# Kernel optimization log

Measured on AMD Instinct MI355X. Metric: run time of the kernel, lower is better.

## Reference

```python
import jax, jax.numpy as jnp
import numpy as np

B, T, C, H = 4, 2048, 1024, 16
D = C // H  # head_dim = 64


def setup_inputs() -> dict:
    key = jax.random.key(0)
    k1, k2, k3 = jax.random.split(key, 3)
    x = jax.random.normal(k1, (B, T, C), dtype=jnp.float32)
    w_attn = jax.random.normal(k2, (C, 3 * C), dtype=jnp.float32) * (1.0 / np.sqrt(C))
    b_attn = jnp.zeros((3 * C,), dtype=jnp.float32)
    w_proj = jax.random.normal(k3, (C, C), dtype=jnp.float32) * (1.0 / np.sqrt(C))
    b_proj = jnp.zeros((C,), dtype=jnp.float32)
    return {"x": x, "w_attn": w_attn, "b_attn": b_attn, "w_proj": w_proj, "b_proj": b_proj}


def reference(x, w_attn, b_attn, w_proj, b_proj):
    Bx, Tx, Cx = x.shape
    qkv = x @ w_attn + b_attn                      # (B, T, 3C)
    q, k, v = jnp.split(qkv, 3, axis=2)
    # (B, T, C) -> (B, H, T, D)
    q = q.reshape(Bx, Tx, H, D).transpose(0, 2, 1, 3)
    k = k.reshape(Bx, Tx, H, D).transpose(0, 2, 1, 3)
    v = v.reshape(Bx, Tx, H, D).transpose(0, 2, 1, 3)
    scores = jnp.einsum('bhqd,bhkd->bhqk', q, k) / jnp.sqrt(jnp.float32(D))
    causal = jnp.tril(jnp.ones((Tx, Tx), dtype=bool))
    scores = jnp.where(causal[None, None], scores, jnp.float32(-jnp.inf))
    probs = jax.nn.softmax(scores, axis=-1)
    out = jnp.einsum('bhqk,bhkd->bhqd', probs, v)  # (B, H, T, D)
    out = out.transpose(0, 2, 1, 3).reshape(Bx, Tx, Cx)
    return out @ w_proj + b_proj
```

## Files before the change

### kernel.cpp

```cpp
#include <hip/hip_runtime.h>

#define AS1 __attribute__((address_space(1)))
#define AS3 __attribute__((address_space(3)))

using bf16x8  = __attribute__((ext_vector_type(8))) __bf16;
using floatx4 = __attribute__((ext_vector_type(4))) float;

#define SCQ 0.18033688f

__device__ inline ushort f2b(float f) {
    __bf16 h = (__bf16)f;
    return __builtin_bit_cast(ushort, h);
}

__device__ inline float fexp2(float x) {
    float r;
    asm("v_exp_f32 %0, %1" : "=v"(r) : "v"(x));
    return r;
}

__device__ inline unsigned cvtpk_bf16(float lo, float hi) {
    unsigned r;
    asm("v_cvt_pk_bf16_f32 %0, %1, %2" : "=v"(r) : "v"(lo), "v"(hi));
    return r;
}
__device__ inline void plswap32(unsigned& a, unsigned& b) {
    asm("v_permlane32_swap_b32 %0, %1" : "+v"(a), "+v"(b));
}
__device__ inline void plswap16(unsigned& a, unsigned& b) {
    asm("v_permlane16_swap_b32 %0, %1" : "+v"(a), "+v"(b));
}

__device__ inline bf16x8 pack_swap(floatx4 ej0, floatx4 ej1) {
    unsigned x0 = cvtpk_bf16(ej0[0], ej0[1]);
    unsigned x1 = cvtpk_bf16(ej0[2], ej0[3]);
    unsigned y0 = cvtpk_bf16(ej1[0], ej1[1]);
    unsigned y1 = cvtpk_bf16(ej1[2], ej1[3]);
    plswap32(x0, y0); plswap16(x0, y0);
    plswap32(x1, y1); plswap16(x1, y1);
    union { unsigned u[4]; bf16x8 v; } ua;
    ua.u[0] = x0; ua.u[1] = x1; ua.u[2] = y0; ua.u[3] = y1;
    return ua.v;
}

__global__ void k_prep(const float* __restrict__ x, ushort* __restrict__ xb,
                       const float* __restrict__ wa, ushort* __restrict__ waT,
                       const float* __restrict__ wp, ushort* __restrict__ wpT)
{
    __shared__ float tile[32][33];
    int blk = blockIdx.x;
    if (blk < 8192) {
        int i = (blk * 256 + threadIdx.x) * 4;
        float4 v = *(const float4*)(x + i);
        ushort4 o;
        o.x = f2b(v.x); o.y = f2b(v.y); o.z = f2b(v.z); o.w = f2b(v.w);
        *(ushort4*)(xb + i) = o;
        return;
    }
    const float* in; ushort* out; int R, Ncol, bx, by; float scale; int scale_cols;
    if (blk < 11264) {
        int idx = blk - 8192;
        in = wa; out = waT; R = 1024; Ncol = 3072;
        bx = idx % 96; by = idx / 96; scale = SCQ; scale_cols = 1024;
    } else {
        int idx = blk - 11264;
        in = wp; out = wpT; R = 1024; Ncol = 1024;
        bx = idx % 32; by = idx / 32; scale = 1.0f; scale_cols = 0;
    }
    int tx = threadIdx.x & 31, ty = threadIdx.x >> 5;
    int c0 = bx * 32, r0 = by * 32;
    for (int i = 0; i < 32; i += 8)
        tile[ty + i][tx] = in[(size_t)(r0 + ty + i) * Ncol + c0 + tx];
    __syncthreads();
    for (int i = 0; i < 32; i += 8) {
        int n = c0 + ty + i;
        float v = tile[tx][ty + i];
        if (n < scale_cols) v *= scale;
        out[(size_t)n * R + r0 + tx] = f2b(v);
    }
}

__device__ inline void xcd_swizzle(int& bx, int& by) {
    int gx = gridDim.x, lin = blockIdx.x + gx * blockIdx.y;
    int nwg = gx * gridDim.y;
    int swz = (lin & 7) * (nwg >> 3) + (lin >> 3);
    bx = swz % gx; by = swz / gx;
}

__global__ __launch_bounds__(256, 2) void k_gemm_bt(
    const ushort* __restrict__ A, const ushort* __restrict__ Bt,
    const float* __restrict__ bias, float* __restrict__ outv,
    int M, int N, int K)
{
    __shared__ __align__(16) ushort As[128 * 64];
    __shared__ __align__(16) ushort Bs[128 * 64];
    int tid = threadIdx.x;
    int bxs, bys; xcd_swizzle(bxs, bys);
    int m0 = bys * 128, n0 = bxs * 128;
    int lane = tid & 63;
    int wm = (tid >> 7) * 64;
    int wn = ((tid >> 6) & 1) * 64;
    int lr = lane & 15, quad = lane >> 4;

    floatx4 acc[4][4] = {};
    const ushort* ags[4]; const ushort* bgs[4]; int sdst[4];
    #pragma unroll
    for (int it = 0; it < 4; ++it) {
        int slot = tid + 256 * it;
        int row = slot >> 3, ch = slot & 7;
        ags[it] = A  + (size_t)(m0 + row) * K + ch * 8;
        bgs[it] = Bt + (size_t)(n0 + row) * K + ch * 8;
        sdst[it] = slot * 8;
    }

    for (int kt = 0; kt < K; kt += 64) {
        #pragma unroll
        for (int it = 0; it < 4; ++it) {
            __builtin_amdgcn_global_load_lds((const AS1 unsigned int*)(ags[it] + kt),
                                             (AS3 unsigned int*)&As[sdst[it]], 16, 0, 0);
            __builtin_amdgcn_global_load_lds((const AS1 unsigned int*)(bgs[it] + kt),
                                             (AS3 unsigned int*)&Bs[sdst[it]], 16, 0, 0);
        }
        asm volatile("s_waitcnt vmcnt(0)" ::: "memory");
        __syncthreads();
        bf16x8 af[4][2], bf[4][2];
        #pragma unroll
        for (int i = 0; i < 4; ++i) {
            af[i][0] = *(const bf16x8*)&As[(wm + 16 * i + lr) * 64 + quad * 8];
            af[i][1] = *(const bf16x8*)&As[(wm + 16 * i + lr) * 64 + 32 + quad * 8];
        }
        #pragma unroll
        for (int j = 0; j < 4; ++j) {
            bf[j][0] = *(const bf16x8*)&Bs[(wn + 16 * j + lr) * 64 + quad * 8];
            bf[j][1] = *(const bf16x8*)&Bs[(wn + 16 * j + lr) * 64 + 32 + quad * 8];
        }
        #pragma unroll
        for (int i = 0; i < 4; ++i)
            #pragma unroll
            for (int j = 0; j < 4; ++j) {
                acc[i][j] = __builtin_amdgcn_mfma_f32_16x16x32_bf16(af[i][0], bf[j][0], acc[i][j], 0, 0, 0);
                acc[i][j] = __builtin_amdgcn_mfma_f32_16x16x32_bf16(af[i][1], bf[j][1], acc[i][j], 0, 0, 0);
            }
        __syncthreads();
    }

    #pragma unroll
    for (int j = 0; j < 4; ++j) {
        int col = n0 + wn + 16 * j + lr;
        float bv = bias[col];
        #pragma unroll
        for (int i = 0; i < 4; ++i) {
            int row = m0 + wm + 16 * i + quad * 4;
            #pragma unroll
            for (int r = 0; r < 4; ++r)
                outv[(size_t)(row + r) * N + col] = acc[i][j][r] + bv;
        }
    }
}

__global__ __launch_bounds__(256, 2) void k_gemm_qkv(
    const ushort* __restrict__ A, const ushort* __restrict__ Bt,
    const float* __restrict__ bias, ushort* __restrict__ qkv, ushort* __restrict__ vt)
{
    constexpr int K = 1024;
    __shared__ __align__(16) ushort As[128 * 64];
    __shared__ __align__(16) ushort Bs[128 * 64];
    int tid = threadIdx.x;
    int bxs, bys; xcd_swizzle(bxs, bys);
    int m0 = bys * 128, n0 = bxs * 128;
    int lane = tid & 63;
    int wm = (tid >> 7) * 64;
    int wn = ((tid >> 6) & 1) * 64;
    int lr = lane & 15, quad = lane >> 4;

    floatx4 acc[4][4] = {};
    const ushort* ags[4]; const ushort* bgs[4]; int sdst[4];
    #pragma unroll
    for (int it = 0; it < 4; ++it) {
        int slot = tid + 256 * it;
        int row = slot >> 3, ch = slot & 7;
        ags[it] = A  + (size_t)(m0 + row) * K + ch * 8;
        bgs[it] = Bt + (size_t)(n0 + row) * K + ch * 8;
        sdst[it] = slot * 8;
    }

    for (int kt = 0; kt < K; kt += 64) {
        #pragma unroll
        for (int it = 0; it < 4; ++it) {
            __builtin_amdgcn_global_load_lds((const AS1 unsigned int*)(ags[it] + kt),
                                             (AS3 unsigned int*)&As[sdst[it]], 16, 0, 0);
            __builtin_amdgcn_global_load_lds((const AS1 unsigned int*)(bgs[it] + kt),
                                             (AS3 unsigned int*)&Bs[sdst[it]], 16, 0, 0);
        }
        asm volatile("s_waitcnt vmcnt(0)" ::: "memory");
        __syncthreads();
        bf16x8 af[4][2], bf[4][2];
        #pragma unroll
        for (int i = 0; i < 4; ++i) {
            af[i][0] = *(const bf16x8*)&As[(wm + 16 * i + lr) * 64 + quad * 8];
            af[i][1] = *(const bf16x8*)&As[(wm + 16 * i + lr) * 64 + 32 + quad * 8];
        }
        #pragma unroll
        for (int j = 0; j < 4; ++j) {
            bf[j][0] = *(const bf16x8*)&Bs[(wn + 16 * j + lr) * 64 + quad * 8];
            bf[j][1] = *(const bf16x8*)&Bs[(wn + 16 * j + lr) * 64 + 32 + quad * 8];
        }
        #pragma unroll
        for (int i = 0; i < 4; ++i)
            #pragma unroll
            for (int j = 0; j < 4; ++j) {
                acc[i][j] = __builtin_amdgcn_mfma_f32_16x16x32_bf16(af[i][0], bf[j][0], acc[i][j], 0, 0, 0);
                acc[i][j] = __builtin_amdgcn_mfma_f32_16x16x32_bf16(af[i][1], bf[j][1], acc[i][j], 0, 0, 0);
            }
        __syncthreads();
    }

    int bb = m0 >> 11;
    #pragma unroll
    for (int j = 0; j < 4; ++j) {
        int col = n0 + wn + 16 * j + lr;
        float bv = bias[col];
        if (col < 1024) bv *= SCQ;
        if (col < 2048) {
            #pragma unroll
            for (int i = 0; i < 4; ++i) {
                int row = m0 + wm + 16 * i + quad * 4;
                #pragma unroll
                for (int r = 0; r < 4; ++r)
                    qkv[(size_t)(row + r) * 2048 + col] = f2b(acc[i][j][r] + bv);
            }
        } else {
            int h = (col - 2048) >> 6, d = (col - 2048) & 63;
            ushort* vbase = vt + ((size_t)(bb * 16 + h) * 64 + d) * 2048;
            #pragma unroll
            for (int i = 0; i < 4; ++i) {
                int t0 = (m0 + wm + 16 * i + quad * 4) & 2047;
                ushort4 pk;
                ((ushort*)&pk)[0] = f2b(acc[i][j][0] + bv);
                ((ushort*)&pk)[1] = f2b(acc[i][j][1] + bv);
                ((ushort*)&pk)[2] = f2b(acc[i][j][2] + bv);
                ((ushort*)&pk)[3] = f2b(acc[i][j][3] + bv);
                *(ushort4*)&vbase[t0] = pk;
            }
        }
    }
}

__device__ __forceinline__ void attn_tile(
    const ushort* __restrict__ Kb, const ushort* __restrict__ Vb,
    bf16x8 aq0, bf16x8 aq1, bf16x8 ones,
    floatx4 (&o)[4], floatx4& lacc,
    int kt, int ktd, int qrow, int lr, int quad, int c0, int c1)
{
    floatx4 s[4];
    __builtin_amdgcn_s_setprio(1);
    #pragma unroll
    for (int j = 0; j < 4; ++j) {
        const ushort* kr = &Kb[(16 * j + lr) * 64];
        bf16x8 bk0 = *(const bf16x8*)(kr + c0);
        bf16x8 bk1 = *(const bf16x8*)(kr + c1);
        floatx4 z = {};
        s[j] = __builtin_amdgcn_mfma_f32_16x16x32_bf16(bk0, aq0, z, 0, 0, 0);
        s[j] = __builtin_amdgcn_mfma_f32_16x16x32_bf16(bk1, aq1, s[j], 0, 0, 0);
    }
    __builtin_amdgcn_s_setprio(0);
    floatx4 e[4];
    if (kt == ktd) {
        int qa = qrow + lr;
        #pragma unroll
        for (int j = 0; j < 4; ++j)
            #pragma unroll
            for (int r = 0; r < 4; ++r)
                e[j][r] = ((kt * 64 + 16 * j + quad * 4 + r) > qa) ? 0.f : fexp2(s[j][r]);
    } else {
        #pragma unroll
        for (int j = 0; j < 4; ++j)
            #pragma unroll
            for (int r = 0; r < 4; ++r)
                e[j][r] = fexp2(s[j][r]);
    }
    bf16x8 ap0 = pack_swap(e[0], e[1]);
    bf16x8 ap1 = pack_swap(e[2], e[3]);
    __builtin_amdgcn_s_setprio(1);
    lacc = __builtin_amdgcn_mfma_f32_16x16x32_bf16(ap0, ones, lacc, 0, 0, 0);
    lacc = __builtin_amdgcn_mfma_f32_16x16x32_bf16(ap1, ones, lacc, 0, 0, 0);
    #pragma unroll
    for (int jd = 0; jd < 4; ++jd) {
        const ushort* vr = &Vb[(16 * jd + lr) * 64];
        bf16x8 bv0 = *(const bf16x8*)(vr + c0);
        bf16x8 bv1 = *(const bf16x8*)(vr + c1);
        o[jd] = __builtin_amdgcn_mfma_f32_16x16x32_bf16(ap0, bv0, o[jd], 0, 0, 0);
        o[jd] = __builtin_amdgcn_mfma_f32_16x16x32_bf16(ap1, bv1, o[jd], 0, 0, 0);
    }
    __builtin_amdgcn_s_setprio(0);
}

__global__ __launch_bounds__(512, 4) void k_attn(const ushort* __restrict__ qkv,
                                                 const ushort* __restrict__ vt,
                                                 ushort* __restrict__ out)
{
    constexpr int T = 2048, SQK = 2048, C = 1024;
    __shared__ __align__(16) ushort Ks[4][64 * 64];
    __shared__ __align__(16) ushort Vs[4][64 * 64];
    int tid = threadIdx.x;
    int lane = tid & 63, wave = tid >> 6;
    int lr = lane & 15, quad = lane >> 4, lk = quad * 8;

    int lin = blockIdx.x + 8 * blockIdx.y;
    int qt  = lin >> 6;
    int bh  = lin & 63;
    int b = bh >> 4, h = bh & 15;
    size_t base = (size_t)b * T * SQK;
    const ushort* kg0 = qkv + base + 1024 + h * 64;
    const ushort* vg0 = vt + (size_t)bh * 64 * 2048;

    int srow = tid >> 3;
    int sg   = (tid & 7) ^ (srow & 7);
    int sdst = tid * 8;
    const ushort* kgs = kg0 + (size_t)srow * SQK + sg * 8;
    const ushort* vgs = vg0 + (size_t)srow * 2048 + sg * 8;

    bf16x8 ones;
    #pragma unroll
    for (int i = 0; i < 8; ++i) ones[i] = (__bf16)1.0f;
    int c0 = (quad ^ (lr & 7)) * 8;
    int c1 = ((4 + quad) ^ (lr & 7)) * 8;

    int qtA = qt, qtB = 15 - qt;
    int qrowA = qtA * 128 + wave * 16;
    int qrowB = qtB * 128 + wave * 16;
    int ktdA = qrowA >> 6, ktdB = qrowB >> 6;
    const ushort* qpA = qkv + base + (size_t)(qrowA + lr) * SQK + h * 64;
    const ushort* qpB = qkv + base + (size_t)(qrowB + lr) * SQK + h * 64;
    bf16x8 aqA0 = *(const bf16x8*)(qpA + lk);
    bf16x8 aqA1 = *(const bf16x8*)(qpA + 32 + lk);
    bf16x8 aqB0 = *(const bf16x8*)(qpB + lk);
    bf16x8 aqB1 = *(const bf16x8*)(qpB + 32 + lk);
    floatx4 oA[4] = {}, oB[4] = {};
    floatx4 laccA = {}, laccB = {};
    int ktmax = 2 * qtB + 1;

    #pragma unroll
    for (int p = 0; p < 3; ++p) {
        __builtin_amdgcn_global_load_lds((const AS1 unsigned int*)(kgs + (size_t)p * 64 * SQK),
                                         (AS3 unsigned int*)&Ks[p][sdst], 16, 0, 0);
        __builtin_amdgcn_global_load_lds((const AS1 unsigned int*)(vgs + p * 64),
                                         (AS3 unsigned int*)&Vs[p][sdst], 16, 0, 0);
    }

    for (int kt = 0; kt <= ktmax; ++kt) {
        __syncthreads();
        if (kt + 3 <= ktmax) {
            int bidx = (kt + 3) & 3;
            __builtin_amdgcn_global_load_lds((const AS1 unsigned int*)(kgs + (size_t)(kt + 3) * 64 * SQK),
                                             (AS3 unsigned int*)&Ks[bidx][sdst], 16, 0, 0);
            __builtin_amdgcn_global_load_lds((const AS1 unsigned int*)(vgs + (kt + 3) * 64),
                                             (AS3 unsigned int*)&Vs[bidx][sdst], 16, 0, 0);
            asm volatile("s_waitcnt vmcnt(6)" ::: "memory");
        } else if (kt + 2 <= ktmax) {
            asm volatile("s_waitcnt vmcnt(4)" ::: "memory");
        } else if (kt + 1 <= ktmax) {
            asm volatile("s_waitcnt vmcnt(2)" ::: "memory");
        } else {
            asm volatile("s_waitcnt vmcnt(0)" ::: "memory");
        }
        __syncthreads();

        const ushort* Kb = Ks[kt & 3];
        const ushort* Vb = Vs[kt & 3];
        if (kt <= ktdB)
            attn_tile(Kb, Vb, aqB0, aqB1, ones, oB, laccB, kt, ktdB, qrowB, lr, quad, c0, c1);
        if (kt <= ktdA)
            attn_tile(Kb, Vb, aqA0, aqA1, ones, oA, laccA, kt, ktdA, qrowA, lr, quad, c0, c1);
    }

    #pragma unroll
    for (int r = 0; r < 4; ++r) {
        float invA = 1.0f / laccA[r];
        float invB = 1.0f / laccB[r];
        int rowA = b * T + qrowA + quad * 4 + r;
        int rowB = b * T + qrowB + quad * 4 + r;
        #pragma unroll
        for (int jd = 0; jd < 4; ++jd) {
            out[(size_t)rowA * C + h * 64 + 16 * jd + lr] = f2b(oA[jd][r] * invA);
            out[(size_t)rowB * C + h * 64 + 16 * jd + lr] = f2b(oB[jd][r] * invB);
        }
    }
}

extern "C" void kernel_launch(void* const* d_in, const int* in_sizes, int n_in,
                              void* d_out, int out_size, void* d_ws, size_t ws_size,
                              hipStream_t stream) {
    const float* x      = (const float*)d_in[0];
    const float* w_attn = (const float*)d_in[1];
    const float* b_attn = (const float*)d_in[2];
    const float* w_proj = (const float*)d_in[3];
    const float* b_proj = (const float*)d_in[4];
    float* out = (float*)d_out;

    constexpr int Bb = 4, T = 2048, C = 1024;
    constexpr int M = Bb * T;

    ushort* xb  = (ushort*)d_ws;
    ushort* waT = xb  + (size_t)M * C;
    ushort* wpT = waT + (size_t)3 * C * C;
    ushort* qkv = wpT + (size_t)C * C;
    ushort* vt  = qkv + (size_t)M * 2 * C;
    ushort* ao  = vt  + (size_t)64 * 64 * T;

    k_prep<<<12288, 256, 0, stream>>>(x, xb, w_attn, waT, w_proj, wpT);
    k_gemm_qkv<<<dim3(3 * C / 128, M / 128), 256, 0, stream>>>(xb, waT, b_attn, qkv, vt);
    k_attn<<<dim3(8, Bb * 16), 512, 0, stream>>>(qkv, vt, ao);
    k_gemm_bt<<<dim3(C / 128, M / 128), 256, 0, stream>>>(ao, wpT, b_proj, out, M, C, C);
}
```

Baseline: 235.6 us.

## Double-buffer GEMM LDS tiles and lighten attention loop barriers

Both projection GEMMs now hold two LDS buffers for A and B tiles. A prologue loads the first tile, and each iteration issues the global-to-LDS loads for the next K tile before the current tile's MFMAs, so memory traffic overlaps with compute. The MFMA block is raised to higher wave priority with s_setprio. In the attention loop, the two full __syncthreads calls become raw s_barrier asm, one with an lgkmcnt wait, to drop extra fence waits. LDS use per block doubles, which could limit occupancy, and the loop relies on __syncthreads draining vmcnt before the prefetched buffer is read.

Result: no change. 239.0 us (+1.4%).

```diff
diff --git a/kernel.cpp b/kernel.cpp
--- a/kernel.cpp
+++ b/kernel.cpp
@@ -30,6 +30,9 @@
 __device__ inline void plswap16(unsigned& a, unsigned& b) {
     asm("v_permlane16_swap_b32 %0, %1" : "+v"(a), "+v"(b));
 }
+
+#define BARRIER_A() asm volatile("s_waitcnt lgkmcnt(0)\n\ts_barrier" ::: "memory")
+#define BARRIER_B() asm volatile("s_barrier" ::: "memory")
 
 __device__ inline bf16x8 pack_swap(floatx4 ej0, floatx4 ej1) {
     unsigned x0 = cvtpk_bf16(ej0[0], ej0[1]);
@@ -92,8 +95,8 @@
     const float* __restrict__ bias, float* __restrict__ outv,
     int M, int N, int K)
 {
-    __shared__ __align__(16) ushort As[128 * 64];
-    __shared__ __align__(16) ushort Bs[128 * 64];
+    __shared__ __align__(16) ushort As[2][128 * 64];
+    __shared__ __align__(16) ushort Bs[2][128 * 64];
     int tid = threadIdx.x;
     int bxs, bys; xcd_swizzle(bxs, bys);
     int m0 = bys * 128, n0 = bxs * 128;
@@ -113,27 +116,41 @@
         sdst[it] = slot * 8;
     }
 
+    #pragma unroll
+    for (int it = 0; it < 4; ++it) {
+        __builtin_amdgcn_global_load_lds((const AS1 unsigned int*)(ags[it]),
+                                         (AS3 unsigned int*)&As[0][sdst[it]], 16, 0, 0);
+        __builtin_amdgcn_global_load_lds((const AS1 unsigned int*)(bgs[it]),
+                                         (AS3 unsigned int*)&Bs[0][sdst[it]], 16, 0, 0);
+    }
+    __syncthreads();
+
+    int cur = 0;
     for (int kt = 0; kt < K; kt += 64) {
-        #pragma unroll
-        for (int it = 0; it < 4; ++it) {
-            __builtin_amdgcn_global_load_lds((const AS1 unsigned int*)(ags[it] + kt),
-                                             (AS3 unsigned int*)&As[sdst[it]], 16, 0, 0);
-            __builtin_amdgcn_global_load_lds((const AS1 unsigned int*)(bgs[it] + kt),
-                                             (AS3 unsigned int*)&Bs[sdst[it]], 16, 0, 0);
-        }
-        asm volatile("s_waitcnt vmcnt(0)" ::: "memory");
-        __syncthreads();
+        if (kt + 64 < K) {
+            #pragma unroll
+            for (int it = 0; it < 4; ++it) {
+                __builtin_amdgcn_global_load_lds((const AS1 unsigned int*)(ags[it] + kt + 64),
+                                                 (AS3 unsigned int*)&As[cur ^ 1][sdst[it]], 16, 0, 0);
+                __builtin_amdgcn_global_load_lds((const AS1 unsigned int*)(bgs[it] + kt + 64),
+                                                 (AS3 unsigned int*)&Bs[cur ^ 1][sdst[it]], 16, 0, 0);
+            }
+        }
+        const ushort* Ab = As[cur];
+        const ushort* Bb = Bs[cur];
         bf16x8 af[4][2], bf[4][2];
         #pragma unroll
         for (int i = 0; i < 4; ++i) {
-            af[i][0] = *(const bf16x8*)&As[(wm + 16 * i + lr) * 64 + quad * 8];
-            af[i][1] = *(const bf16x8*)&As[(wm + 16 * i + lr) * 64 + 32 + quad * 8];
+            af[i][0] = *(const bf16x8*)&Ab[(wm + 16 * i + lr) * 64 + quad * 8];
+            af[i][1] = *(const bf16x8*)&Ab[(wm + 16 * i + lr) * 64 + 32 + quad * 8];
         }
         #pragma unroll
         for (int j = 0; j < 4; ++j) {
-            bf[j][0] = *(const bf16x8*)&Bs[(wn + 16 * j + lr) * 64 + quad * 8];
-            bf[j][1] = *(const bf16x8*)&Bs[(wn + 16 * j + lr) * 64 + 32 + quad * 8];
-        }
+            bf[j][0] = *(const bf16x8*)&Bs[cur][(wn + 16 * j + lr) * 64 + quad * 8];
+            bf[j][1] = *(const bf16x8*)&Bs[cur][(wn + 16 * j + lr) * 64 + 32 + quad * 8];
+        }
+        (void)Bb;
+        __builtin_amdgcn_s_setprio(1);
         #pragma unroll
         for (int i = 0; i < 4; ++i)
             #pragma unroll
@@ -141,7 +158,9 @@
                 acc[i][j] = __builtin_amdgcn_mfma_f32_16x16x32_bf16(af[i][0], bf[j][0], acc[i][j], 0, 0, 0);
                 acc[i][j] = __builtin_amdgcn_mfma_f32_16x16x32_bf16(af[i][1], bf[j][1], acc[i][j], 0, 0, 0);
             }
+        __builtin_amdgcn_s_setprio(0);
         __syncthreads();
+        cur ^= 1;
     }
 
     #pragma unroll
@@ -163,8 +182,8 @@
     const float* __restrict__ bias, ushort* __restrict__ qkv, ushort* __restrict__ vt)
 {
     constexpr int K = 1024;
-    __shared__ __align__(16) ushort As[128 * 64];
-    __shared__ __align__(16) ushort Bs[128 * 64];
+    __shared__ __align__(16) ushort As[2][128 * 64];
+    __shared__ __align__(16) ushort Bs[2][128 * 64];
     int tid = threadIdx.x;
     int bxs, bys; xcd_swizzle(bxs, bys);
     int m0 = bys * 128, n0 = bxs * 128;
@@ -184,27 +203,38 @@
         sdst[it] = slot * 8;
     }
 
+    #pragma unroll
+    for (int it = 0; it < 4; ++it) {
+        __builtin_amdgcn_global_load_lds((const AS1 unsigned int*)(ags[it]),
+                                         (AS3 unsigned int*)&As[0][sdst[it]], 16, 0, 0);
+        __builtin_amdgcn_global_load_lds((const AS1 unsigned int*)(bgs[it]),
+                                         (AS3 unsigned int*)&Bs[0][sdst[it]], 16, 0, 0);
+    }
+    __syncthreads();
+
+    int cur = 0;
     for (int kt = 0; kt < K; kt += 64) {
-        #pragma unroll
-        for (int it = 0; it < 4; ++it) {
-            __builtin_amdgcn_global_load_lds((const AS1 unsigned int*)(ags[it] + kt),
-                                             (AS3 unsigned int*)&As[sdst[it]], 16, 0, 0);
-            __builtin_amdgcn_global_load_lds((const AS1 unsigned int*)(bgs[it] + kt),
-                                             (AS3 unsigned int*)&Bs[sdst[it]], 16, 0, 0);
-        }
-        asm volatile("s_waitcnt vmcnt(0)" ::: "memory");
-        __syncthreads();
+        if (kt + 64 < K) {
+            #pragma unroll
+            for (int it = 0; it < 4; ++it) {
+                __builtin_amdgcn_global_load_lds((const AS1 unsigned int*)(ags[it] + kt + 64),
+                                                 (AS3 unsigned int*)&As[cur ^ 1][sdst[it]], 16, 0, 0);
+                __builtin_amdgcn_global_load_lds((const AS1 unsigned int*)(bgs[it] + kt + 64),
+                                                 (AS3 unsigned int*)&Bs[cur ^ 1][sdst[it]], 16, 0, 0);
+            }
+        }
         bf16x8 af[4][2], bf[4][2];
         #pragma unroll
         for (int i = 0; i < 4; ++i) {
-            af[i][0] = *(const bf16x8*)&As[(wm + 16 * i + lr) * 64 + quad * 8];
-            af[i][1] = *(const bf16x8*)&As[(wm + 16 * i + lr) * 64 + 32 + quad * 8];
+            af[i][0] = *(const bf16x8*)&As[cur][(wm + 16 * i + lr) * 64 + quad * 8];
+            af[i][1] = *(const bf16x8*)&As[cur][(wm + 16 * i + lr) * 64 + 32 + quad * 8];
         }
         #pragma unroll
         for (int j = 0; j < 4; ++j) {
-            bf[j][0] = *(const bf16x8*)&Bs[(wn + 16 * j + lr) * 64 + quad * 8];
-            bf[j][1] = *(const bf16x8*)&Bs[(wn + 16 * j + lr) * 64 + 32 + quad * 8];
-        }
+            bf[j][0] = *(const bf16x8*)&Bs[cur][(wn + 16 * j + lr) * 64 + quad * 8];
+            bf[j][1] = *(const bf16x8*)&Bs[cur][(wn + 16 * j + lr) * 64 + 32 + quad * 8];
+        }
+        __builtin_amdgcn_s_setprio(1);
         #pragma unroll
         for (int i = 0; i < 4; ++i)
             #pragma unroll
@@ -212,7 +242,9 @@
                 acc[i][j] = __builtin_amdgcn_mfma_f32_16x16x32_bf16(af[i][0], bf[j][0], acc[i][j], 0, 0, 0);
                 acc[i][j] = __builtin_amdgcn_mfma_f32_16x16x32_bf16(af[i][1], bf[j][1], acc[i][j], 0, 0, 0);
             }
+        __builtin_amdgcn_s_setprio(0);
         __syncthreads();
+        cur ^= 1;
     }
 
     int bb = m0 >> 11;
@@ -349,7 +381,7 @@
     }
 
     for (int kt = 0; kt <= ktmax; ++kt) {
-        __syncthreads();
+        BARRIER_A();
         if (kt + 3 <= ktmax) {
             int bidx = (kt + 3) & 3;
             __builtin_amdgcn_global_load_lds((const AS1 unsigned int*)(kgs + (size_t)(kt + 3) * 64 * SQK),
@@ -364,7 +396,7 @@
         } else {
             asm volatile("s_waitcnt vmcnt(0)" ::: "memory");
         }
-        __syncthreads();
+        BARRIER_B();
 
         const ushort* Kb = Ks[kt & 3];
         const ushort* Vb = Vs[kt & 3];
```
